# Optimization experiments

Hardware: AMD Instinct MI355X
Metric: run time of the kernel (lower is better)

Reference implementation:

```python
import jax, jax.numpy as jnp
import numpy as np

H = 70  # LSTM hidden size (hard-coded in module)

def _lstm_cell(x, h, c, Wih, Whh, bih, bhh):
    # torch gate order: i, f, g, o
    gates = x @ Wih.T + h @ Whh.T + bih + bhh  # [B, 4H]
    i, f, g, o = jnp.split(gates, 4, axis=-1)
    i = jax.nn.sigmoid(i); f = jax.nn.sigmoid(f)
    g = jnp.tanh(g);       o = jax.nn.sigmoid(o)
    c_new = f * c + i * g
    h_new = o * jnp.tanh(c_new)
    return h_new, c_new

def setup_inputs() -> dict:
    key = jax.random.key(0)
    ks = jax.random.split(key, 16)
    T, B, D = 512, 4096, 64
    s_in = 1.0 / np.sqrt(H)
    def u(k, shape):
        return jax.random.uniform(k, shape, jnp.float32, -s_in, s_in)
    return {
        "data_in": jax.random.normal(ks[0], (T, B, D), jnp.float32),
        "batch_dim": B,
        "W_ih0": u(ks[1], (4 * H, D)),  "W_hh0": u(ks[2], (4 * H, H)),
        "b_ih0": u(ks[3], (4 * H,)),    "b_hh0": u(ks[4], (4 * H,)),
        "W_ih1": u(ks[5], (4 * H, H)),  "W_hh1": u(ks[6], (4 * H, H)),
        "b_ih1": u(ks[7], (4 * H,)),    "b_hh1": u(ks[8], (4 * H,)),
        "W1": u(ks[9], (50, H)), "b1": u(ks[10], (50,)),
        "W2": u(ks[11], (1, 50)), "b2": u(ks[12], (1,)),
    }

def reference(data_in, batch_dim, W_ih0, W_hh0, b_ih0, b_hh0,
              W_ih1, W_hh1, b_ih1, b_hh1, W1, b1, W2, b2):
    B = data_in.shape[1]
    z = jnp.zeros((B, H), data_in.dtype)
    def step(carry, x_t):
        h0, c0, h1, c1 = carry
        h0, c0 = _lstm_cell(x_t, h0, c0, W_ih0, W_hh0, b_ih0, b_hh0)
        h1, c1 = _lstm_cell(h0, h1, c1, W_ih1, W_hh1, b_ih1, b_hh1)
        return (h0, c0, h1, c1), None
    (h0, c0, h1, c1), _ = jax.lax.scan(step, (z, z, z, z), data_in)
    # head uses h_n of the last (second) layer
    out = jax.nn.relu(h1 @ W1.T + b1)
    out = jax.nn.sigmoid(out @ W2.T + b2)  # [B, 1]
    return out
```

## Files before the change

### kernel.cpp

```cpp
#include <hip/hip_runtime.h>
#include <stdint.h>

#define T_STEPS 512
#define BATCH   4096
#define DIN     64
#define HID     70
#define KDIM    160
#define KS      5
#define RB      16
#define WAVES   16
#define NTHR    (WAVES*64)
#define NTILES  18
#define ASP     232
#define H1S     72

typedef __bf16 bf16x8 __attribute__((ext_vector_type(8)));
typedef float  f32x4  __attribute__((ext_vector_type(4)));
typedef unsigned short ushort_t;

#define NLOG2E   (-1.44269504088896340736f)
#define TWOLOG2E ( 2.88539008177792681472f)

__device__ __forceinline__ ushort_t f2bf(float f) {
    uint32_t u = __float_as_uint(f);
    u += 0x7fffu + ((u >> 16) & 1u);
    return (ushort_t)(u >> 16);
}
__device__ __forceinline__ float sigm(float x) {
    return __builtin_amdgcn_rcpf(1.0f + __expf(-x));
}

__device__ __forceinline__ float cell(const f32x4 a, float& cc) {
    float u0 = __builtin_amdgcn_exp2f(a[0]);
    float u1 = __builtin_amdgcn_exp2f(a[1]);
    float v  = __builtin_amdgcn_exp2f(fminf(a[2], 88.0f));
    float u3 = __builtin_amdgcn_exp2f(a[3]);
    float ig = (v - 1.0f) * __builtin_amdgcn_rcpf((1.0f + u0) * (1.0f + v));
    float f_ = __builtin_amdgcn_rcpf(1.0f + u1);
    float cn = fmaf(f_, cc, ig);
    cc = cn;
    float w  = __builtin_amdgcn_exp2f(fminf(cn * TWOLOG2E, 88.0f));
    return (w - 1.0f) * __builtin_amdgcn_rcpf((1.0f + u3) * (1.0f + w));
}

__global__ void prep_kernel(const float* __restrict__ Wih0, const float* __restrict__ Whh0,
                            const float* __restrict__ bih0, const float* __restrict__ bhh0,
                            const float* __restrict__ Wih1, const float* __restrict__ Whh1,
                            const float* __restrict__ bih1, const float* __restrict__ bhh1,
                            ushort_t* __restrict__ W0p, ushort_t* __restrict__ W1p,
                            float* __restrict__ B0p, float* __restrict__ B1p) {
    int idx = blockIdx.x * 256 + threadIdx.x;
    const int n = NTILES * 16 * KDIM;
    if (idx < n) {
        int row = idx / KDIM, k = idx - row * KDIM;
        int t = row >> 4, m = row & 15;
        int gate = m & 3, h = 4*t + (m >> 2);
        float sc = (gate == 2) ? TWOLOG2E : NLOG2E;
        float v0 = 0.f, v1 = 0.f;
        if (h < HID) {
            int g = gate * HID + h;
            if (k < 64)        v0 = Wih0[g*64 + k];
            else if (k < 134)  v0 = Whh0[g*HID + (k - 64)];
            if (k < 70)                   v1 = Wih1[g*HID + k];
            else if (k >= 80 && k < 150)  v1 = Whh1[g*HID + (k - 80)];
        }
        W0p[idx] = f2bf(sc * v0);
        W1p[idx] = f2bf(sc * v1);
    }
    if (idx < NTILES*16) {
        int t = idx >> 4, m = idx & 15;
        int gate = m & 3, h = 4*t + (m >> 2);
        float sc = (gate == 2) ? TWOLOG2E : NLOG2E;
        float s0 = 0.f, s1 = 0.f;
        if (h < HID) {
            int g = gate * HID + h;
            s0 = sc * (bih0[g] + bhh0[g]);
            s1 = sc * (bih1[g] + bhh1[g]);
        }
        B0p[idx] = s0; B1p[idx] = s1;
    }
}

__global__ __launch_bounds__(NTHR, 4) void lstm_kernel(
    const float* __restrict__ x,
    const ushort_t* __restrict__ W0p, const ushort_t* __restrict__ W1p,
    const float* __restrict__ B0p, const float* __restrict__ B1p,
    const float* __restrict__ W1h, const float* __restrict__ b1h,
    const float* __restrict__ W2h, const float* __restrict__ b2h,
    float* __restrict__ out)
{
    __shared__ alignas(16) ushort_t P[2][RB*ASP];
    __shared__ float h1f[RB*H1S];
    __shared__ float mid[RB*50];

    const int tid  = threadIdx.x;
    const int wave = tid >> 6;
    const int lane = tid & 63;
    const int n15  = lane & 15;
    const int q    = lane >> 4;
    const int blk  = blockIdx.x;
    const bool isL0 = (wave & 1);
    const int lw   = wave >> 1;
    const bool cw3 = (lw < 2);
    const int t0   = cw3 ? lw*3 : (6 + (lw-2)*2);
    const int hcol0 = t0*4 + q;

    const ushort_t* __restrict__ Wp = isL0 ? W0p : W1p;
    const float*    __restrict__ Bp = isL0 ? B0p : B1p;

    bf16x8 wA[3][KS];
    f32x4  bias[3];
    bias[2] = f32x4{0.f, 0.f, 0.f, 0.f};
    {
        const int r0 = (t0*16 + n15)*KDIM + q*8;
        const int r1 = ((t0+1)*16 + n15)*KDIM + q*8;
        #pragma unroll
        for (int ks = 0; ks < KS; ks++) {
            wA[0][ks] = *(const bf16x8*)(Wp + r0 + ks*32);
            wA[1][ks] = *(const bf16x8*)(Wp + r1 + ks*32);
        }
        bias[0] = *(const f32x4*)(Bp + t0*16 + q*4);
        bias[1] = *(const f32x4*)(Bp + (t0+1)*16 + q*4);
        if (cw3) {
            const int r2 = ((t0+2)*16 + n15)*KDIM + q*8;
            #pragma unroll
            for (int ks = 0; ks < KS; ks++)
                wA[2][ks] = *(const bf16x8*)(Wp + r2 + ks*32);
            bias[2] = *(const f32x4*)(Bp + (t0+2)*16 + q*4);
        }
    }
    const int kbase = (isL0 ? 0 : 64) + n15*ASP + q*8;
    const int hoff  = isL0 ? 64 : 144;

    float cc[3] = {0.f, 0.f, 0.f};

    for (int i = tid; i < 2*RB*ASP; i += NTHR) (&P[0][0])[i] = 0;

    const bool xl   = (wave >= 12);
    const int  xt   = (wave - 12)*64 + lane;
    const int  xrow = (xt >> 4) & 15;
    const int  xcol = (xt & 15) * 4;
    const float* xptr = x + ((size_t)blk*RB + xrow)*DIN + xcol;

    f32x4 x0v, x1v, xcur;
    if (xl) {
        x0v  = *(const f32x4*)(xptr);
        x1v  = *(const f32x4*)(xptr + (size_t)1*(BATCH*DIN));
        xcur = *(const f32x4*)(xptr + (size_t)2*(BATCH*DIN));
    }
    __syncthreads();
    if (xl) {
        uint32_t a0, a1, b0, b1;
        asm("v_cvt_pk_bf16_f32 %0, %1, %2" : "=v"(a0) : "v"(x0v[0]), "v"(x0v[1]));
        asm("v_cvt_pk_bf16_f32 %0, %1, %2" : "=v"(a1) : "v"(x0v[2]), "v"(x0v[3]));
        asm("v_cvt_pk_bf16_f32 %0, %1, %2" : "=v"(b0) : "v"(x1v[0]), "v"(x1v[1]));
        asm("v_cvt_pk_bf16_f32 %0, %1, %2" : "=v"(b1) : "v"(x1v[2]), "v"(x1v[3]));
        uint2 pa; pa.x = a0; pa.y = a1;
        uint2 pb; pb.x = b0; pb.y = b1;
        *(uint2*)(&P[1][xrow*ASP + xcol]) = pa;
        *(uint2*)(&P[0][xrow*ASP + xcol]) = pb;
    }
    __syncthreads();

    auto gemm = [&](const ushort_t* bp, float* hv) __attribute__((always_inline)) {
        bf16x8 b[KS];
        #pragma unroll
        for (int ks = 0; ks < KS; ks++)
            b[ks] = *(const bf16x8*)(bp + ks*32);
        f32x4 a0 = bias[0], a1 = bias[1], a2 = bias[2];
        #pragma unroll
        for (int ks = 0; ks < KS; ks++) {
            a0 = __builtin_amdgcn_mfma_f32_16x16x32_bf16(wA[0][ks], b[ks], a0, 0,0,0);
            a1 = __builtin_amdgcn_mfma_f32_16x16x32_bf16(wA[1][ks], b[ks], a1, 0,0,0);
            if (cw3)
                a2 = __builtin_amdgcn_mfma_f32_16x16x32_bf16(wA[2][ks], b[ks], a2, 0,0,0);
        }
        hv[0] = cell(a0, cc[0]);
        hv[1] = cell(a1, cc[1]);
        if (cw3) hv[2] = cell(a2, cc[2]);
    };
    auto storeh = [&](ushort_t* hp, const float* hv) __attribute__((always_inline)) {
        uint32_t pk01;
        asm("v_cvt_pk_bf16_f32 %0, %1, %2" : "=v"(pk01) : "v"(hv[0]), "v"(hv[1]));
        hp[0] = (ushort_t)pk01;
        hp[4] = (ushort_t)(pk01 >> 16);
        if (cw3) {
            uint32_t pk2;
            asm("v_cvt_pk_bf16_f32 %0, %1, %2" : "=v"(pk2) : "v"(hv[2]), "v"(hv[2]));
            hp[8] = (ushort_t)pk2;
        }
    };

    if (isL0) {
        float hv[3];
        gemm(&P[1][kbase], hv);
        storeh(&P[0][n15*ASP + 64 + hcol0], hv);
    }
    __syncthreads();

    auto phase = [&](const int cur, const int p) __attribute__((always_inline)) {
        const int nxt = cur ^ 1;
        f32x4 xn;
        if (xl) {
            int tn = p + 3; if (tn > T_STEPS-1) tn = T_STEPS-1;
            xn = *(const f32x4*)(xptr + (size_t)tn*(BATCH*DIN));
        }
        float hv[3];
        gemm(&P[cur][kbase], hv);
        if (xl) {
            uint32_t s0, s1;
            asm("v_cvt_pk_bf16_f32 %0, %1, %2" : "=v"(s0) : "v"(xcur[0]), "v"(xcur[1]));
            asm("v_cvt_pk_bf16_f32 %0, %1, %2" : "=v"(s1) : "v"(xcur[2]), "v"(xcur[3]));
            uint2 pv; pv.x = s0; pv.y = s1;
            *(uint2*)(&P[nxt][xrow*ASP + xcol]) = pv;
            xcur = xn;
        }
        storeh(&P[nxt][n15*ASP + hoff + hcol0], hv);
        asm volatile("s_waitcnt lgkmcnt(0)" ::: "memory");
        __builtin_amdgcn_s_barrier();
        asm volatile("" ::: "memory");
    };

    #pragma unroll 1
    for (int p = 0; p < T_STEPS - 2; p += 2) {
        phase(0, p);
        phase(1, p + 1);
    }
    phase(0, T_STEPS - 2);

    if (!isL0) {
        float hv[3];
        gemm(&P[1][kbase], hv);
        float* hd = &h1f[n15*H1S + hcol0];
        hd[0] = hv[0];
        hd[4] = hv[1];
        if (cw3) hd[8] = hv[2];
    }
    __syncthreads();

    for (int uu = tid; uu < RB*50; uu += NTHR) {
        const int r = uu / 50, j = uu - r*50;
        float s = b1h[j];
        const float* wgt = W1h + j*HID;
        const float* hh  = h1f + r*H1S;
        #pragma unroll 7
        for (int k = 0; k < HID; k++) s += wgt[k]*hh[k];
        mid[uu] = fmaxf(s, 0.0f);
    }
    __syncthreads();
    if (tid < RB) {
        float s = b2h[0];
        const float* m = mid + tid*50;
        #pragma unroll 10
        for (int j = 0; j < 50; j++) s += W2h[j]*m[j];
        out[blk*RB + tid] = sigm(s);
    }
}

extern "C" void kernel_launch(void* const* d_in, const int* in_sizes, int n_in,
                              void* d_out, int out_size, void* d_ws, size_t ws_size,
                              hipStream_t stream) {
    (void)in_sizes; (void)n_in; (void)out_size; (void)ws_size;
    const float* x    = (const float*)d_in[0];
    const float* Wih0 = (const float*)d_in[2];
    const float* Whh0 = (const float*)d_in[3];
    const float* bih0 = (const float*)d_in[4];
    const float* bhh0 = (const float*)d_in[5];
    const float* Wih1 = (const float*)d_in[6];
    const float* Whh1 = (const float*)d_in[7];
    const float* bih1 = (const float*)d_in[8];
    const float* bhh1 = (const float*)d_in[9];
    const float* W1h  = (const float*)d_in[10];
    const float* b1h  = (const float*)d_in[11];
    const float* W2h  = (const float*)d_in[12];
    const float* b2h  = (const float*)d_in[13];

    char* ws = (char*)d_ws;
    ushort_t* W0p = (ushort_t*)ws;
    ushort_t* W1p = (ushort_t*)(ws + 92160);
    float*    B0p = (float*)(ws + 184320);
    float*    B1p = (float*)(ws + 185472);

    prep_kernel<<<180, 256, 0, stream>>>(Wih0, Whh0, bih0, bhh0,
                                         Wih1, Whh1, bih1, bhh1,
                                         W0p, W1p, B0p, B1p);
    lstm_kernel<<<BATCH/RB, NTHR, 0, stream>>>(x, W0p, W1p, B0p, B1p,
                                               W1h, b1h, W2h, b2h, (float*)d_out);
}
```

Baseline: 1.054 ms.

## Rebalance LSTM block to 12 waves with uniform 3-tile work and permuted hidden layout

Cuts the block from 16 to 12 waves so every wave owns exactly three 16-row gate tiles, removing the uneven 3/2-tile split and its branches. The hidden-state columns in the weight packing are permuted so each wave's three outputs land contiguously in LDS and can be written with packed 32-bit stores. The x loader moves onto threads 384-639, which share waves with the compute work. The custom barrier is replaced by __syncthreads, and launch_bounds drops the minimum occupancy hint. Fewer waves means less latency hiding, and the x-load work now falls on compute waves.

```diff
diff --git a/kernel.cpp b/kernel.cpp
--- a/kernel.cpp
+++ b/kernel.cpp
@@ -8,9 +8,10 @@
 #define KDIM    160
 #define KS      5
 #define RB      16
-#define WAVES   16
+#define WAVES   12
 #define NTHR    (WAVES*64)
 #define NTILES  18
+#define CH      3
 #define ASP     232
 #define H1S     72
 
@@ -59,10 +60,19 @@
         float v0 = 0.f, v1 = 0.f;
         if (h < HID) {
             int g = gate * HID + h;
-            if (k < 64)        v0 = Wih0[g*64 + k];
-            else if (k < 134)  v0 = Whh0[g*HID + (k - 64)];
-            if (k < 70)                   v1 = Wih1[g*HID + k];
-            else if (k >= 80 && k < 150)  v1 = Whh1[g*HID + (k - 80)];
+            if (k < 64) {
+                v0 = Wih0[g*64 + k];
+            } else if (k < 136) {
+                int u = k - 64, hh = 4*(u % 18) + u/18;
+                if (hh < HID) v0 = Whh0[g*HID + hh];
+            }
+            if (k < 72) {
+                int hh = 4*(k % 18) + k/18;
+                if (hh < HID) v1 = Wih1[g*HID + hh];
+            } else if (k >= 80 && k < 152) {
+                int u = k - 80, hh = 4*(u % 18) + u/18;
+                if (hh < HID) v1 = Whh1[g*HID + hh];
+            }
         }
         W0p[idx] = f2bf(sc * v0);
         W1p[idx] = f2bf(sc * v1);
@@ -81,7 +91,7 @@
     }
 }
 
-__global__ __launch_bounds__(NTHR, 4) void lstm_kernel(
+__global__ __launch_bounds__(NTHR) void lstm_kernel(
     const float* __restrict__ x,
     const ushort_t* __restrict__ W0p, const ushort_t* __restrict__ W1p,
     const float* __restrict__ B0p, const float* __restrict__ B1p,
@@ -99,46 +109,34 @@
     const int n15  = lane & 15;
     const int q    = lane >> 4;
     const int blk  = blockIdx.x;
-    const bool isL0 = (wave & 1);
-    const int lw   = wave >> 1;
-    const bool cw3 = (lw < 2);
-    const int t0   = cw3 ? lw*3 : (6 + (lw-2)*2);
-    const int hcol0 = t0*4 + q;
+    const bool isL0 = (wave >= 6);
+    const int lw   = isL0 ? wave - 6 : wave;
+    const int t0   = lw * CH;
 
     const ushort_t* __restrict__ Wp = isL0 ? W0p : W1p;
     const float*    __restrict__ Bp = isL0 ? B0p : B1p;
 
-    bf16x8 wA[3][KS];
-    f32x4  bias[3];
-    bias[2] = f32x4{0.f, 0.f, 0.f, 0.f};
-    {
-        const int r0 = (t0*16 + n15)*KDIM + q*8;
-        const int r1 = ((t0+1)*16 + n15)*KDIM + q*8;
+    bf16x8 wA[CH][KS];
+    f32x4  bias[CH];
+    #pragma unroll
+    for (int c = 0; c < CH; c++) {
+        const int rowb = ((t0 + c)*16 + n15)*KDIM + q*8;
         #pragma unroll
-        for (int ks = 0; ks < KS; ks++) {
-            wA[0][ks] = *(const bf16x8*)(Wp + r0 + ks*32);
-            wA[1][ks] = *(const bf16x8*)(Wp + r1 + ks*32);
-        }
-        bias[0] = *(const f32x4*)(Bp + t0*16 + q*4);
-        bias[1] = *(const f32x4*)(Bp + (t0+1)*16 + q*4);
-        if (cw3) {
-            const int r2 = ((t0+2)*16 + n15)*KDIM + q*8;
-            #pragma unroll
-            for (int ks = 0; ks < KS; ks++)
-                wA[2][ks] = *(const bf16x8*)(Wp + r2 + ks*32);
-            bias[2] = *(const f32x4*)(Bp + (t0+2)*16 + q*4);
-        }
+        for (int ks = 0; ks < KS; ks++)
+            wA[c][ks] = *(const bf16x8*)(Wp + rowb + ks*32);
+        bias[c] = *(const f32x4*)(Bp + (t0 + c)*16 + q*4);
     }
     const int kbase = (isL0 ? 0 : 64) + n15*ASP + q*8;
-    const int hoff  = isL0 ? 64 : 144;
-
-    float cc[3] = {0.f, 0.f, 0.f};
+    const int hpos  = n15*ASP + (isL0 ? 64 : 144) + q*18 + t0;
+    const bool evenT = ((t0 & 1) == 0);
+
+    float cc[CH] = {0.f, 0.f, 0.f};
 
     for (int i = tid; i < 2*RB*ASP; i += NTHR) (&P[0][0])[i] = 0;
 
-    const bool xl   = (wave >= 12);
-    const int  xt   = (wave - 12)*64 + lane;
-    const int  xrow = (xt >> 4) & 15;
+    const int  xt   = tid - 384;
+    const bool xl   = (xt >= 0) && (xt < 256);
+    const int  xrow = xt >> 4;
     const int  xcol = (xt & 15) * 4;
     const float* xptr = x + ((size_t)blk*RB + xrow)*DIN + xcol;
 
@@ -172,29 +170,31 @@
         for (int ks = 0; ks < KS; ks++) {
             a0 = __builtin_amdgcn_mfma_f32_16x16x32_bf16(wA[0][ks], b[ks], a0, 0,0,0);
             a1 = __builtin_amdgcn_mfma_f32_16x16x32_bf16(wA[1][ks], b[ks], a1, 0,0,0);
-            if (cw3)
-                a2 = __builtin_amdgcn_mfma_f32_16x16x32_bf16(wA[2][ks], b[ks], a2, 0,0,0);
+            a2 = __builtin_amdgcn_mfma_f32_16x16x32_bf16(wA[2][ks], b[ks], a2, 0,0,0);
         }
         hv[0] = cell(a0, cc[0]);
         hv[1] = cell(a1, cc[1]);
-        if (cw3) hv[2] = cell(a2, cc[2]);
+        hv[2] = cell(a2, cc[2]);
     };
-    auto storeh = [&](ushort_t* hp, const float* hv) __attribute__((always_inline)) {
-        uint32_t pk01;
-        asm("v_cvt_pk_bf16_f32 %0, %1, %2" : "=v"(pk01) : "v"(hv[0]), "v"(hv[1]));
-        hp[0] = (ushort_t)pk01;
-        hp[4] = (ushort_t)(pk01 >> 16);
-        if (cw3) {
-            uint32_t pk2;
-            asm("v_cvt_pk_bf16_f32 %0, %1, %2" : "=v"(pk2) : "v"(hv[2]), "v"(hv[2]));
-            hp[8] = (ushort_t)pk2;
+    auto storeh = [&](ushort_t* Pn, const float* hv) __attribute__((always_inline)) {
+        uint32_t pkA, pkB;
+        if (evenT) {
+            asm("v_cvt_pk_bf16_f32 %0, %1, %2" : "=v"(pkA) : "v"(hv[0]), "v"(hv[1]));
+            asm("v_cvt_pk_bf16_f32 %0, %1, %2" : "=v"(pkB) : "v"(hv[2]), "v"(hv[2]));
+            *(uint32_t*)(Pn + hpos) = pkA;
+            Pn[hpos + 2] = (ushort_t)pkB;
+        } else {
+            asm("v_cvt_pk_bf16_f32 %0, %1, %2" : "=v"(pkA) : "v"(hv[0]), "v"(hv[0]));
+            asm("v_cvt_pk_bf16_f32 %0, %1, %2" : "=v"(pkB) : "v"(hv[1]), "v"(hv[2]));
+            Pn[hpos] = (ushort_t)pkA;
+            *(uint32_t*)(Pn + hpos + 1) = pkB;
         }
     };
 
     if (isL0) {
-        float hv[3];
+        float hv[CH];
         gemm(&P[1][kbase], hv);
-        storeh(&P[0][n15*ASP + 64 + hcol0], hv);
+        storeh(&P[0][0], hv);
     }
     __syncthreads();
 
@@ -205,7 +205,7 @@
             int tn = p + 3; if (tn > T_STEPS-1) tn = T_STEPS-1;
             xn = *(const f32x4*)(xptr + (size_t)tn*(BATCH*DIN));
         }
-        float hv[3];
+        float hv[CH];
         gemm(&P[cur][kbase], hv);
         if (xl) {
             uint32_t s0, s1;
@@ -215,10 +215,8 @@
             *(uint2*)(&P[nxt][xrow*ASP + xcol]) = pv;
             xcur = xn;
         }
-        storeh(&P[nxt][n15*ASP + hoff + hcol0], hv);
-        asm volatile("s_waitcnt lgkmcnt(0)" ::: "memory");
-        __builtin_amdgcn_s_barrier();
-        asm volatile("" ::: "memory");
+        storeh(&P[nxt][0], hv);
+        __syncthreads();
     };
 
     #pragma unroll 1
@@ -229,12 +227,12 @@
     phase(0, T_STEPS - 2);
 
     if (!isL0) {
-        float hv[3];
+        float hv[CH];
         gemm(&P[1][kbase], hv);
-        float* hd = &h1f[n15*H1S + hcol0];
+        float* hd = &h1f[n15*H1S + t0*4 + q];
         hd[0] = hv[0];
         hd[4] = hv[1];
-        if (cw3) hd[8] = hv[2];
+        hd[8] = hv[2];
     }
     __syncthreads();
 
```

Measured after the change: 1.032 ms. 1.02x faster.
